# Kernel tuning notes

Measured on AMD Instinct MI355X. Metric: run time of the kernel, lower is better.

The kernel has to match this reference:

```python
import jax, jax.numpy as jnp
import numpy as np

N_NODES = 100000
N_EDGES = 1600000
D_FEAT = 128


def setup_inputs() -> dict:
    key = jax.random.key(0)
    k1, k2, k3 = jax.random.split(key, 3)
    feat = jax.random.normal(k1, (N_NODES, D_FEAT), dtype=jnp.float32)
    src = jax.random.randint(k2, (N_EDGES,), 0, N_NODES, dtype=jnp.int32)
    dst = jax.random.randint(k3, (N_EDGES,), 0, N_NODES, dtype=jnp.int32)
    return {"feat": feat, "src": src, "dst": dst}


def reference(feat, src, dst):
    n = feat.shape[0]
    ones = jnp.ones(src.shape[0], dtype=feat.dtype)
    # out-degree of each node (as message source), clamped to >= 1
    deg_o = jnp.clip(jax.ops.segment_sum(ones, src, num_segments=n), 1.0)
    norm_l = deg_o ** -0.5  # [N]
    feat_scaled = feat * norm_l[:, None]
    # copy_u + sum aggregation: gather from src, scatter-add to dst
    agg = jax.ops.segment_sum(feat_scaled[src], dst, num_segments=n)
    # in-degree normalization on destination side
    deg_i = jnp.clip(jax.ops.segment_sum(ones, dst, num_segments=n), 1.0)
    norm_r = deg_i ** -0.5
    return agg * norm_r[:, None]
```

## Files before the change

kernel.cpp:

```cpp
#include <hip/hip_runtime.h>
#include <hip/hip_fp16.h>

#define D_FEAT      128
#define SCAN_B      1024
#define S_BIN       512
#define BUCKET_BITS 7
#define BUCKET_SZ   128
#define NB_MAX      1024
#define SORT_CAP    6144

typedef float f32x4 __attribute__((ext_vector_type(4)));

__global__ void binhist2_kernel(const int* __restrict__ src, const int* __restrict__ dst,
                                int* __restrict__ part2, int n_edges, int nb, int N2,
                                int slice_len) {
    __shared__ int hd[NB_MAX];
    __shared__ int hs[NB_MAX];
    int s = blockIdx.x;
    for (int i = threadIdx.x; i < nb; i += blockDim.x) { hd[i] = 0; hs[i] = 0; }
    __syncthreads();
    int beg = s * slice_len;
    int end = beg + slice_len; if (end > n_edges) end = n_edges;
    for (int i = beg + threadIdx.x; i < end; i += blockDim.x) {
        atomicAdd(&hd[dst[i] >> BUCKET_BITS], 1);
        atomicAdd(&hs[src[i] >> BUCKET_BITS], 1);
    }
    __syncthreads();
    for (int b = threadIdx.x; b < nb; b += blockDim.x) {
        part2[(size_t)b * S_BIN + s] = hd[b];
        part2[(size_t)(N2 + b * S_BIN) + s] = hs[b];
    }
}

__global__ __launch_bounds__(SCAN_B) void scan1_kernel(int* __restrict__ data,
        int* __restrict__ bsum, int n) {
    __shared__ int sh[SCAN_B];
    int t = threadIdx.x;
    int g = blockIdx.x * SCAN_B + t;
    int v = (g < n) ? data[g] : 0;
    sh[t] = v;
    __syncthreads();
    for (int d = 1; d < SCAN_B; d <<= 1) {
        int x = (t >= d) ? sh[t - d] : 0;
        __syncthreads();
        sh[t] += x;
        __syncthreads();
    }
    if (g < n) data[g] = sh[t] - v;
    if (t == SCAN_B - 1) bsum[blockIdx.x] = sh[t];
}

__global__ __launch_bounds__(SCAN_B) void scan2_kernel(int* __restrict__ bsum, int nb) {
    __shared__ int sh[SCAN_B];
    int t = threadIdx.x;
    int v = (t < nb) ? bsum[t] : 0;
    sh[t] = v;
    __syncthreads();
    for (int d = 1; d < SCAN_B; d <<= 1) {
        int x = (t >= d) ? sh[t - d] : 0;
        __syncthreads();
        sh[t] += x;
        __syncthreads();
    }
    if (t < nb) bsum[t] = sh[t] - v;
}

__global__ void binscatter2_kernel(const int* __restrict__ src, const int* __restrict__ dst,
                                   const int* __restrict__ loff, const int* __restrict__ bsum,
                                   int* __restrict__ colp, unsigned char* __restrict__ colp_src,
                                   int n_edges, int nb, int N2, int slice_len) {
    __shared__ int cd[NB_MAX];
    __shared__ int cs[NB_MAX];
    int s = blockIdx.x;
    for (int b = threadIdx.x; b < nb; b += blockDim.x) {
        size_t iD = (size_t)b * S_BIN + s;
        size_t iS = (size_t)N2 + (size_t)b * S_BIN + s;
        cd[b] = loff[iD] + bsum[iD >> 10];
        cs[b] = loff[iS] + bsum[iS >> 10] - n_edges;
    }
    __syncthreads();
    int beg = s * slice_len;
    int end = beg + slice_len; if (end > n_edges) end = n_edges;
    for (int i = beg + threadIdx.x; i < end; i += blockDim.x) {
        int d = dst[i], sv = src[i];
        int pD = atomicAdd(&cd[d >> BUCKET_BITS], 1);
        colp[pD] = sv | ((d & (BUCKET_SZ - 1)) << 20);
        int pS = atomicAdd(&cs[sv >> BUCKET_BITS], 1);
        colp_src[pS] = (unsigned char)(sv & (BUCKET_SZ - 1));
    }
}

__global__ __launch_bounds__(256) void sortcount_kernel(
        int* __restrict__ colp, const unsigned char* __restrict__ colp_src,
        const int* __restrict__ loff, const int* __restrict__ bsum,
        int* __restrict__ node_off, float* __restrict__ norm_l,
        int n_nodes, int n_edges, int nb, int N2) {
    __shared__ int buf[SORT_CAP];
    __shared__ int cnt[BUCKET_SZ];
    __shared__ int sa[BUCKET_SZ];
    __shared__ int sb[BUCKET_SZ];
    int tid = threadIdx.x;

    if ((int)blockIdx.x >= nb) {
        int b = blockIdx.x - nb;
        size_t iA = (size_t)N2 + (size_t)b * S_BIN;
        int beg = loff[iA] + bsum[iA >> 10] - n_edges;
        int end;
        if (b + 1 < nb) {
            size_t iB = (size_t)N2 + (size_t)(b + 1) * S_BIN;
            end = loff[iB] + bsum[iB >> 10] - n_edges;
        } else end = n_edges;
        if (tid < BUCKET_SZ) cnt[tid] = 0;
        __syncthreads();
        for (int i = beg + tid; i < end; i += blockDim.x)
            atomicAdd(&cnt[colp_src[i]], 1);
        __syncthreads();
        int node0 = b << BUCKET_BITS;
        int bn = n_nodes - node0; if (bn > BUCKET_SZ) bn = BUCKET_SZ;
        if (tid < bn) {
            int c = cnt[tid]; if (c < 1) c = 1;
            norm_l[node0 + tid] = rsqrtf((float)c);
        }
        return;
    }

    int b = blockIdx.x;
    size_t iA = (size_t)b * S_BIN;
    int beg = loff[iA] + bsum[iA >> 10];
    int end;
    if (b + 1 < nb) {
        size_t iB = (size_t)(b + 1) * S_BIN;
        end = loff[iB] + bsum[iB >> 10];
    } else end = n_edges;
    int m = end - beg;
    if (tid < BUCKET_SZ) cnt[tid] = 0;
    __syncthreads();
    for (int i = tid; i < m; i += blockDim.x) {
        int v = colp[beg + i];
        if (i < SORT_CAP) buf[i] = v;
        atomicAdd(&cnt[(v >> 20) & (BUCKET_SZ - 1)], 1);
    }
    __syncthreads();
    int* rp = sa; int* wp = sb;
    if (tid < BUCKET_SZ) sa[tid] = cnt[tid];
    __syncthreads();
    for (int d = 1; d < BUCKET_SZ; d <<= 1) {
        if (tid < BUCKET_SZ) wp[tid] = rp[tid] + (tid >= d ? rp[tid - d] : 0);
        __syncthreads();
        int* t = rp; rp = wp; wp = t;
    }
    int node0 = b << BUCKET_BITS;
    int bn = n_nodes - node0; if (bn > BUCKET_SZ) bn = BUCKET_SZ;
    if (tid < BUCKET_SZ) {
        int ex = rp[tid] - cnt[tid];
        wp[tid] = ex;
        if (tid < bn) node_off[node0 + tid] = beg + ex;
    }
    if (b == nb - 1 && tid == 0) node_off[n_nodes] = end;
    __syncthreads();
    int mm = m < SORT_CAP ? m : SORT_CAP;
    for (int i = tid; i < mm; i += blockDim.x) {
        int v = buf[i];
        int p = atomicAdd(&wp[(v >> 20) & (BUCKET_SZ - 1)], 1);
        colp[beg + p] = v & 0xFFFFF;
    }
}

__global__ void convert_kernel(const float* __restrict__ feat, const float* __restrict__ norm_l,
                               __half* __restrict__ feat16, int n_nodes) {
    int t = blockIdx.x * blockDim.x + threadIdx.x;
    int total = n_nodes * (D_FEAT / 8);
    if (t >= total) return;
    float nl = norm_l[t >> 4];
    const f32x4* fp = (const f32x4*)feat + (size_t)t * 2;
    f32x4 a = __builtin_nontemporal_load(fp);
    f32x4 b = __builtin_nontemporal_load(fp + 1);
    __half2 h0 = __floats2half2_rn(a.x * nl, a.y * nl);
    __half2 h1 = __floats2half2_rn(a.z * nl, a.w * nl);
    __half2 h2 = __floats2half2_rn(b.x * nl, b.y * nl);
    __half2 h3 = __floats2half2_rn(b.z * nl, b.w * nl);
    uint4 o;
    o.x = *(unsigned int*)&h0; o.y = *(unsigned int*)&h1;
    o.z = *(unsigned int*)&h2; o.w = *(unsigned int*)&h3;
    ((uint4*)feat16)[t] = o;
}

__global__ __launch_bounds__(256) void pull_csr_kernel(
        const __half* __restrict__ feat16, const int* __restrict__ col,
        const int* __restrict__ node_off, float* __restrict__ out, int n_nodes) {
    int lane = threadIdx.x & 63;
    int wid  = (int)(((long long)blockIdx.x * blockDim.x + threadIdx.x) >> 6);
    int h  = lane >> 5;
    int g  = (lane >> 4) & 1;
    int dl = lane & 15;
    int node = wid * 2 + h;
    bool nvalid = node < n_nodes;
    int nsafe = nvalid ? node : n_nodes - 1;
    int s = node_off[nsafe];
    int e = nvalid ? node_off[nsafe + 1] : s;
    int m = e - s;
    int om = __shfl_xor(m, 32, 64);
    int mm = m > om ? m : om;

    float a0=0.f,a1=0.f,a2=0.f,a3=0.f,a4=0.f,a5=0.f,a6=0.f,a7=0.f;
    const uint4* rowb = (const uint4*)feat16;

    for (int base = 0; base < mm; base += 32) {
        int remh = m - base;
        int cl = lane & 31;
        int ci = cl;
        if (ci >= remh) ci = (remh > 0) ? remh - 1 : 0;
        int cv = col[s + base + ci];
        int lim = mm - base; if (lim > 32) lim = 32;
        for (int k = 0; k < lim; k += 2) {
            int srcl = (lane & 32) + k + g;
            int idx = __shfl(cv, srcl, 64);
            if (base + k + g < m) {
                uint4 hv = rowb[((size_t)(unsigned)idx << 4) + dl];
                float2 f;
                f = __half22float2(*(__half2*)&hv.x); a0 += f.x; a1 += f.y;
                f = __half22float2(*(__half2*)&hv.y); a2 += f.x; a3 += f.y;
                f = __half22float2(*(__half2*)&hv.z); a4 += f.x; a5 += f.y;
                f = __half22float2(*(__half2*)&hv.w); a6 += f.x; a7 += f.y;
            }
        }
    }

    a0 += __shfl_xor(a0, 16, 64); a1 += __shfl_xor(a1, 16, 64);
    a2 += __shfl_xor(a2, 16, 64); a3 += __shfl_xor(a3, 16, 64);
    a4 += __shfl_xor(a4, 16, 64); a5 += __shfl_xor(a5, 16, 64);
    a6 += __shfl_xor(a6, 16, 64); a7 += __shfl_xor(a7, 16, 64);

    if (nvalid && g == 0) {
        int c = m < 1 ? 1 : m;
        float nr = rsqrtf((float)c);
        f32x4 o0 = {a0 * nr, a1 * nr, a2 * nr, a3 * nr};
        f32x4 o1 = {a4 * nr, a5 * nr, a6 * nr, a7 * nr};
        f32x4* op = (f32x4*)(out + (size_t)node * D_FEAT) + dl * 2;
        __builtin_nontemporal_store(o0, op);
        __builtin_nontemporal_store(o1, op + 1);
    }
}

extern "C" void kernel_launch(void* const* d_in, const int* in_sizes, int n_in,
                              void* d_out, int out_size, void* d_ws, size_t ws_size,
                              hipStream_t stream) {
    const float* feat = (const float*)d_in[0];
    const int*   src  = (const int*)d_in[1];
    const int*   dst  = (const int*)d_in[2];
    float* out = (float*)d_out;

    const int n_nodes = in_sizes[0] / D_FEAT;
    const int n_edges = in_sizes[1];
    const int nb = (n_nodes + BUCKET_SZ - 1) / BUCKET_SZ;
    const int N2 = nb * S_BIN;
    const int NSCAN = 2 * N2;
    const int sl = (n_edges + S_BIN - 1) / S_BIN;

    auto alignup = [](size_t x) { return (x + 255) & ~(size_t)255; };
    char* p = (char*)d_ws;
    int*    node_off = (int*)p;            p += alignup((size_t)(n_nodes + 1) * 4);
    float*  norm_l   = (float*)p;          p += alignup((size_t)n_nodes * 4);
    int*    part2    = (int*)p;            p += alignup((size_t)NSCAN * 4);
    int*    bsum     = (int*)p;            p += alignup((size_t)SCAN_B * 4);
    int*    colp     = (int*)p;            p += alignup((size_t)n_edges * 4);
    unsigned char* colp_src = (unsigned char*)p; p += alignup((size_t)n_edges);
    __half* feat16   = (__half*)p;

    binhist2_kernel<<<S_BIN, 256, 0, stream>>>(src, dst, part2, n_edges, nb, N2, sl);

    {
        int nsb = (NSCAN + SCAN_B - 1) / SCAN_B;
        scan1_kernel<<<nsb, SCAN_B, 0, stream>>>(part2, bsum, NSCAN);
        scan2_kernel<<<1, SCAN_B, 0, stream>>>(bsum, nsb);
    }

    binscatter2_kernel<<<S_BIN, 256, 0, stream>>>(src, dst, part2, bsum, colp, colp_src,
                                                  n_edges, nb, N2, sl);

    sortcount_kernel<<<2 * nb, 256, 0, stream>>>(colp, colp_src, part2, bsum, node_off,
                                                 norm_l, n_nodes, n_edges, nb, N2);

    {
        int total = n_nodes * (D_FEAT / 8);
        convert_kernel<<<(total + 255) / 256, 256, 0, stream>>>(feat, norm_l, feat16, n_nodes);
    }

    {
        long long waves = ((long long)n_nodes + 1) / 2;
        long long total = waves * 64;
        pull_csr_kernel<<<(int)((total + 255) / 256), 256, 0, stream>>>(feat16, colp, node_off,
                                                                        out, n_nodes);
    }
}
```

Baseline: 248.7 us.

## Use wave-shuffle scans, larger binning blocks, and branchless pull gather

Replaces the shared-memory Hillis-Steele scans with wavefront shuffle scans plus a small per-wave sum array, cutting the many block-wide barriers. Halves the number of edge slices (S_BIN 512 to 256) and runs the histogram and scatter kernels with 1024-thread blocks, which shrinks the partial-count array that must be scanned. The pull kernel now always loads the neighbour row and multiplies by a 0/1 mask instead of branching, with the column index clamped to stay in bounds. In exchange, masked lanes issue redundant row loads, and fewer, larger blocks may reduce parallelism in the binning passes.

New measurement: 227.6 us. 8.5% less time.

```diff
diff --git a/kernel.cpp b/kernel.cpp
--- a/kernel.cpp
+++ b/kernel.cpp
@@ -2,77 +2,102 @@
 #include <hip/hip_fp16.h>
 
 #define D_FEAT      128
-#define SCAN_B      1024
-#define S_BIN       512
+#define S_BIN       256
 #define BUCKET_BITS 7
 #define BUCKET_SZ   128
 #define NB_MAX      1024
 #define SORT_CAP    6144
+#define BIGB        1024
 
 typedef float f32x4 __attribute__((ext_vector_type(4)));
 
-__global__ void binhist2_kernel(const int* __restrict__ src, const int* __restrict__ dst,
-                                int* __restrict__ part2, int n_edges, int nb, int N2,
-                                int slice_len) {
+__global__ __launch_bounds__(BIGB) void binhist2_kernel(
+        const int* __restrict__ src, const int* __restrict__ dst,
+        int* __restrict__ part2, int n_edges, int nb, int N2, int slice_len) {
     __shared__ int hd[NB_MAX];
     __shared__ int hs[NB_MAX];
-    int s = blockIdx.x;
-    for (int i = threadIdx.x; i < nb; i += blockDim.x) { hd[i] = 0; hs[i] = 0; }
+    int s = blockIdx.x, tid = threadIdx.x;
+    for (int i = tid; i < nb; i += BIGB) { hd[i] = 0; hs[i] = 0; }
     __syncthreads();
     int beg = s * slice_len;
     int end = beg + slice_len; if (end > n_edges) end = n_edges;
-    for (int i = beg + threadIdx.x; i < end; i += blockDim.x) {
+    for (int i = beg + tid; i < end; i += BIGB) {
         atomicAdd(&hd[dst[i] >> BUCKET_BITS], 1);
         atomicAdd(&hs[src[i] >> BUCKET_BITS], 1);
     }
     __syncthreads();
-    for (int b = threadIdx.x; b < nb; b += blockDim.x) {
+    for (int b = tid; b < nb; b += BIGB) {
         part2[(size_t)b * S_BIN + s] = hd[b];
         part2[(size_t)(N2 + b * S_BIN) + s] = hs[b];
     }
 }
 
-__global__ __launch_bounds__(SCAN_B) void scan1_kernel(int* __restrict__ data,
+__global__ __launch_bounds__(BIGB) void scan1_kernel(int* __restrict__ data,
         int* __restrict__ bsum, int n) {
-    __shared__ int sh[SCAN_B];
-    int t = threadIdx.x;
-    int g = blockIdx.x * SCAN_B + t;
+    __shared__ int wsum[16];
+    int tid = threadIdx.x;
+    int g = blockIdx.x * BIGB + tid;
+    int lane = tid & 63, w = tid >> 6;
     int v = (g < n) ? data[g] : 0;
-    sh[t] = v;
-    __syncthreads();
-    for (int d = 1; d < SCAN_B; d <<= 1) {
-        int x = (t >= d) ? sh[t - d] : 0;
-        __syncthreads();
-        sh[t] += x;
-        __syncthreads();
-    }
-    if (g < n) data[g] = sh[t] - v;
-    if (t == SCAN_B - 1) bsum[blockIdx.x] = sh[t];
-}
-
-__global__ __launch_bounds__(SCAN_B) void scan2_kernel(int* __restrict__ bsum, int nb) {
-    __shared__ int sh[SCAN_B];
-    int t = threadIdx.x;
-    int v = (t < nb) ? bsum[t] : 0;
-    sh[t] = v;
-    __syncthreads();
-    for (int d = 1; d < SCAN_B; d <<= 1) {
-        int x = (t >= d) ? sh[t - d] : 0;
-        __syncthreads();
-        sh[t] += x;
-        __syncthreads();
-    }
-    if (t < nb) bsum[t] = sh[t] - v;
-}
-
-__global__ void binscatter2_kernel(const int* __restrict__ src, const int* __restrict__ dst,
-                                   const int* __restrict__ loff, const int* __restrict__ bsum,
-                                   int* __restrict__ colp, unsigned char* __restrict__ colp_src,
-                                   int n_edges, int nb, int N2, int slice_len) {
+    int incl = v;
+    #pragma unroll
+    for (int d = 1; d < 64; d <<= 1) {
+        int x = __shfl_up(incl, d, 64);
+        if (lane >= d) incl += x;
+    }
+    if (lane == 63) wsum[w] = incl;
+    __syncthreads();
+    if (w == 0) {
+        int sv = (lane < 16) ? wsum[lane] : 0;
+        #pragma unroll
+        for (int d = 1; d < 16; d <<= 1) {
+            int x = __shfl_up(sv, d, 64);
+            if (lane >= d) sv += x;
+        }
+        if (lane < 16) wsum[lane] = sv;
+    }
+    __syncthreads();
+    int wpre = (w > 0) ? wsum[w - 1] : 0;
+    if (g < n) data[g] = wpre + incl - v;
+    if (tid == BIGB - 1) bsum[blockIdx.x] = wpre + incl;
+}
+
+__global__ __launch_bounds__(BIGB) void scan2_kernel(int* __restrict__ bsum, int nchunks) {
+    __shared__ int wsum[16];
+    int tid = threadIdx.x;
+    int lane = tid & 63, w = tid >> 6;
+    int v = (tid < nchunks) ? bsum[tid] : 0;
+    int incl = v;
+    #pragma unroll
+    for (int d = 1; d < 64; d <<= 1) {
+        int x = __shfl_up(incl, d, 64);
+        if (lane >= d) incl += x;
+    }
+    if (lane == 63) wsum[w] = incl;
+    __syncthreads();
+    if (w == 0) {
+        int sv = (lane < 16) ? wsum[lane] : 0;
+        #pragma unroll
+        for (int d = 1; d < 16; d <<= 1) {
+            int x = __shfl_up(sv, d, 64);
+            if (lane >= d) sv += x;
+        }
+        if (lane < 16) wsum[lane] = sv;
+    }
+    __syncthreads();
+    int wpre = (w > 0) ? wsum[w - 1] : 0;
+    if (tid < nchunks) bsum[tid] = wpre + incl - v;
+}
+
+__global__ __launch_bounds__(BIGB) void binscatter2_kernel(
+        const int* __restrict__ src, const int* __restrict__ dst,
+        const int* __restrict__ loff, const int* __restrict__ bsum,
+        int* __restrict__ colp, unsigned char* __restrict__ colp_src,
+        int n_edges, int nb, int N2, int slice_len) {
     __shared__ int cd[NB_MAX];
     __shared__ int cs[NB_MAX];
-    int s = blockIdx.x;
-    for (int b = threadIdx.x; b < nb; b += blockDim.x) {
+    int s = blockIdx.x, tid = threadIdx.x;
+    for (int b = tid; b < nb; b += BIGB) {
         size_t iD = (size_t)b * S_BIN + s;
         size_t iS = (size_t)N2 + (size_t)b * S_BIN + s;
         cd[b] = loff[iD] + bsum[iD >> 10];
@@ -81,7 +106,7 @@
     __syncthreads();
     int beg = s * slice_len;
     int end = beg + slice_len; if (end > n_edges) end = n_edges;
-    for (int i = beg + threadIdx.x; i < end; i += blockDim.x) {
+    for (int i = beg + tid; i < end; i += BIGB) {
         int d = dst[i], sv = src[i];
         int pD = atomicAdd(&cd[d >> BUCKET_BITS], 1);
         colp[pD] = sv | ((d & (BUCKET_SZ - 1)) << 20);
@@ -187,7 +212,8 @@
 
 __global__ __launch_bounds__(256) void pull_csr_kernel(
         const __half* __restrict__ feat16, const int* __restrict__ col,
-        const int* __restrict__ node_off, float* __restrict__ out, int n_nodes) {
+        const int* __restrict__ node_off, float* __restrict__ out,
+        int n_nodes, int n_edges) {
     int lane = threadIdx.x & 63;
     int wid  = (int)(((long long)blockIdx.x * blockDim.x + threadIdx.x) >> 6);
     int h  = lane >> 5;
@@ -207,22 +233,22 @@
 
     for (int base = 0; base < mm; base += 32) {
         int remh = m - base;
-        int cl = lane & 31;
-        int ci = cl;
+        int ci = lane & 31;
         if (ci >= remh) ci = (remh > 0) ? remh - 1 : 0;
-        int cv = col[s + base + ci];
+        int cidx = s + base + ci;
+        if (cidx >= n_edges) cidx = n_edges - 1;
+        int cv = col[cidx];
         int lim = mm - base; if (lim > 32) lim = 32;
         for (int k = 0; k < lim; k += 2) {
             int srcl = (lane & 32) + k + g;
             int idx = __shfl(cv, srcl, 64);
-            if (base + k + g < m) {
-                uint4 hv = rowb[((size_t)(unsigned)idx << 4) + dl];
-                float2 f;
-                f = __half22float2(*(__half2*)&hv.x); a0 += f.x; a1 += f.y;
-                f = __half22float2(*(__half2*)&hv.y); a2 += f.x; a3 += f.y;
-                f = __half22float2(*(__half2*)&hv.z); a4 += f.x; a5 += f.y;
-                f = __half22float2(*(__half2*)&hv.w); a6 += f.x; a7 += f.y;
-            }
+            uint4 hv = rowb[((size_t)(unsigned)idx << 4) + dl];
+            float wm = (base + k + g < m) ? 1.f : 0.f;
+            float2 f;
+            f = __half22float2(*(__half2*)&hv.x); a0 += wm * f.x; a1 += wm * f.y;
+            f = __half22float2(*(__half2*)&hv.y); a2 += wm * f.x; a3 += wm * f.y;
+            f = __half22float2(*(__half2*)&hv.z); a4 += wm * f.x; a5 += wm * f.y;
+            f = __half22float2(*(__half2*)&hv.w); a6 += wm * f.x; a7 += wm * f.y;
         }
     }
 
@@ -250,33 +276,33 @@
     const int*   dst  = (const int*)d_in[2];
     float* out = (float*)d_out;
 
-    const int n_nodes = in_sizes[0] / D_FEAT;
-    const int n_edges = in_sizes[1];
-    const int nb = (n_nodes + BUCKET_SZ - 1) / BUCKET_SZ;
-    const int N2 = nb * S_BIN;
-    const int NSCAN = 2 * N2;
-    const int sl = (n_edges + S_BIN - 1) / S_BIN;
+    int n_nodes = in_sizes[0] / D_FEAT;
+    int n_edges = in_sizes[1];
+    int nb = (n_nodes + BUCKET_SZ - 1) / BUCKET_SZ;
+    int N2 = nb * S_BIN;
+    int NSCAN = 2 * N2;
+    int sl = (n_edges + S_BIN - 1) / S_BIN;
 
     auto alignup = [](size_t x) { return (x + 255) & ~(size_t)255; };
     char* p = (char*)d_ws;
     int*    node_off = (int*)p;            p += alignup((size_t)(n_nodes + 1) * 4);
     float*  norm_l   = (float*)p;          p += alignup((size_t)n_nodes * 4);
     int*    part2    = (int*)p;            p += alignup((size_t)NSCAN * 4);
-    int*    bsum     = (int*)p;            p += alignup((size_t)SCAN_B * 4);
+    int*    bsum     = (int*)p;            p += alignup((size_t)BIGB * 4);
     int*    colp     = (int*)p;            p += alignup((size_t)n_edges * 4);
     unsigned char* colp_src = (unsigned char*)p; p += alignup((size_t)n_edges);
     __half* feat16   = (__half*)p;
 
-    binhist2_kernel<<<S_BIN, 256, 0, stream>>>(src, dst, part2, n_edges, nb, N2, sl);
+    binhist2_kernel<<<S_BIN, BIGB, 0, stream>>>(src, dst, part2, n_edges, nb, N2, sl);
 
     {
-        int nsb = (NSCAN + SCAN_B - 1) / SCAN_B;
-        scan1_kernel<<<nsb, SCAN_B, 0, stream>>>(part2, bsum, NSCAN);
-        scan2_kernel<<<1, SCAN_B, 0, stream>>>(bsum, nsb);
-    }
-
-    binscatter2_kernel<<<S_BIN, 256, 0, stream>>>(src, dst, part2, bsum, colp, colp_src,
-                                                  n_edges, nb, N2, sl);
+        int nch = (NSCAN + BIGB - 1) / BIGB;
+        scan1_kernel<<<nch, BIGB, 0, stream>>>(part2, bsum, NSCAN);
+        scan2_kernel<<<1, BIGB, 0, stream>>>(bsum, nch);
+    }
+
+    binscatter2_kernel<<<S_BIN, BIGB, 0, stream>>>(src, dst, part2, bsum, colp, colp_src,
+                                                   n_edges, nb, N2, sl);
 
     sortcount_kernel<<<2 * nb, 256, 0, stream>>>(colp, colp_src, part2, bsum, node_off,
                                                  norm_l, n_nodes, n_edges, nb, N2);
@@ -290,6 +316,6 @@
         long long waves = ((long long)n_nodes + 1) / 2;
         long long total = waves * 64;
         pull_csr_kernel<<<(int)((total + 255) / 256), 256, 0, stream>>>(feat16, colp, node_off,
-                                                                        out, n_nodes);
-    }
-}
+                                                                        out, n_nodes, n_edges);
+    }
+}
```
